# Kernel tuning notes

Hardware: AMD Instinct MI355X
Metric: run time of the kernel (lower is better)

The kernel has to match this reference:

```python
import jax, jax.numpy as jnp
import numpy as np

N = 4096
D_IN = 1024
D_OUT = 512
DENSITY = 0.005
LRELU_ALPHA = 0.2  # tf.nn.leaky_relu default


def _make_adj(key):
    # sparse binary adjacency, symmetric, with self-loops (dense 0/1 float mask)
    a = (jax.random.uniform(key, (N, N)) < DENSITY).astype(jnp.float32)
    a = jnp.maximum(a, a.T)
    a = jnp.maximum(a, jnp.eye(N, dtype=jnp.float32))
    return a


def setup_inputs() -> dict:
    key = jax.random.key(0)
    ks = jax.random.split(key, 7)
    x = jax.random.normal(ks[0], (N, D_IN), dtype=jnp.float32)
    adj = _make_adj(ks[1])
    # glorot-ish scales
    Wf = jax.random.normal(ks[2], (D_IN, D_OUT), dtype=jnp.float32) * (1.0 / np.sqrt(D_IN))
    a1 = jax.random.normal(ks[3], (D_OUT, 1), dtype=jnp.float32) * (1.0 / np.sqrt(D_OUT))
    b1 = jnp.zeros((1,), dtype=jnp.float32)
    a2 = jax.random.normal(ks[4], (D_OUT, 1), dtype=jnp.float32) * (1.0 / np.sqrt(D_OUT))
    b2 = jnp.zeros((1,), dtype=jnp.float32)
    W = jax.random.normal(ks[5], (D_IN, D_OUT), dtype=jnp.float32) * (1.0 / np.sqrt(D_IN))
    return {"x": x, "adj": adj, "Wf": Wf, "a1": a1, "b1": b1, "a2": a2, "b2": b2, "W": W}


def reference(x, adj, Wf, a1, b1, a2, b2, W):
    # dropout = 0 (inference) -> identity; coef dropout skipped for determinism
    mask = adj != 0.0
    # conv1d(kernel=1) == pointwise linear
    seq_fts = x @ Wf                      # [N, D_OUT]
    f1 = seq_fts @ a1 + b1                # [N, 1]
    f2 = seq_fts @ a2 + b2                # [N, 1]
    # sparse logits: adj_ij * f1_i + adj_ij * f2_j on edges
    logits = adj * f1 + adj * f2.T        # [N, N]
    lrelu = jnp.where(logits >= 0, logits, LRELU_ALPHA * logits)
    # sparse softmax over edge entries per row
    masked = jnp.where(mask, lrelu, -jnp.inf)
    coefs = jax.nn.softmax(masked, axis=1)
    coefs = jnp.where(mask, coefs, 0.0)
    # symmetrize: (coefs + coefs^T)/2
    coefs = (coefs + coefs.T) * 0.5
    # coefs_I = diag(rowsum^0) = I  (pow(x,0)==1)
    coefs_mat = coefs + jnp.eye(N, dtype=coefs.dtype)
    rowsum = jnp.sum(coefs_mat, axis=1, keepdims=True)   # [N,1], >= 1
    d_inv_sqrt = rowsum ** -0.5
    d_inv_inverse = d_inv_sqrt ** -1.0
    inf_int = jnp.isinf(d_inv_sqrt).astype(jnp.float32)
    d = (d_inv_inverse + inf_int) ** -1.0 - inf_int
    d = jnp.sum(d, axis=1)                # [N]
    d_mat = jnp.diag(d)                   # [N,N] diagonal matrix
    # NOTE: original uses ELEMENTWISE multiply with the diag matrix (faithful):
    support_mat = (coefs_mat * d_mat).T * d_mat   # effectively diagonal
    pre_sup = x @ W                       # [N, D_OUT]
    out = support_mat @ pre_sup           # [N, D_OUT]
    return jax.nn.relu(out)
```

## Files before the change

kernel.cpp:

```cpp
#include <hip/hip_runtime.h>
#include <stdint.h>
#include <math.h>

#define NN 4096
#define DIN 1024
#define DOUT 512
#define ALPHA 0.2f

typedef __attribute__((ext_vector_type(8))) short short8;
typedef __attribute__((ext_vector_type(4))) float f32x4;

__device__ __forceinline__ unsigned short f2bf(float f) {
    uint32_t u = __float_as_uint(f);
    u += 0x7fffu + ((u >> 16) & 1u);
    return (unsigned short)(u >> 16);
}

__device__ __forceinline__ void async16(const void* g, void* l) {
    __builtin_amdgcn_global_load_lds(
        (const __attribute__((address_space(1))) uint32_t*)g,
        (__attribute__((address_space(3))) uint32_t*)l, 16, 0, 0);
}

__global__ __launch_bounds__(256) void k_wa(const float* __restrict__ Wf,
                                            const float* __restrict__ a1,
                                            const float* __restrict__ a2,
                                            float* __restrict__ wa1,
                                            float* __restrict__ wa2) {
    int row  = blockIdx.x * 4 + (threadIdx.x >> 6);
    int lane = threadIdx.x & 63;
    const float* wr = Wf + (size_t)row * DOUT;
    float s1 = 0.f, s2 = 0.f;
    for (int k = lane; k < DOUT; k += 64) {
        float w = wr[k];
        s1 += w * a1[k];
        s2 += w * a2[k];
    }
    for (int off = 32; off; off >>= 1) {
        s1 += __shfl_down(s1, off);
        s2 += __shfl_down(s2, off);
    }
    if (lane == 0) { wa1[row] = s1; wa2[row] = s2; }
}

__global__ __launch_bounds__(256) void k_maskfx(const float* __restrict__ adj,
    const float* __restrict__ x, const float* __restrict__ W,
    const float* __restrict__ wa1, const float* __restrict__ wa2,
    const float* __restrict__ b1, const float* __restrict__ b2,
    float* __restrict__ f1, float* __restrict__ f2,
    unsigned short* __restrict__ xb, unsigned short* __restrict__ wt,
    unsigned short* __restrict__ bits16) {
    int tid = threadIdx.x;
    if (blockIdx.x < 2048) {
        int row0 = blockIdx.x * 2;
        const float4* a0 = (const float4*)(adj + (size_t)row0 * NN);
        const float4* a1v = (const float4*)(adj + (size_t)(row0 + 1) * NN);
        float4 v0 = a0[tid];        float4 v1 = a0[tid + 256];
        float4 v2 = a0[tid + 512];  float4 v3 = a0[tid + 768];
        float4 v4 = a1v[tid];       float4 v5 = a1v[tid + 256];
        float4 v6 = a1v[tid + 512]; float4 v7 = a1v[tid + 768];
        __builtin_amdgcn_sched_barrier(0);
        unsigned int m0 = 0, m1 = 0;
#define MB(M, V, J)                                            \
        M |= (((V).x != 0.f) ? 1u : 0u) << (4 * (J));          \
        M |= (((V).y != 0.f) ? 1u : 0u) << (4 * (J) + 1);      \
        M |= (((V).z != 0.f) ? 1u : 0u) << (4 * (J) + 2);      \
        M |= (((V).w != 0.f) ? 1u : 0u) << (4 * (J) + 3);
        MB(m0, v0, 0) MB(m0, v1, 1) MB(m0, v2, 2) MB(m0, v3, 3)
        MB(m1, v4, 0) MB(m1, v5, 1) MB(m1, v6, 2) MB(m1, v7, 3)
#undef MB
        bits16[(size_t)row0 * 256 + tid]       = (unsigned short)m0;
        bits16[(size_t)row0 * 256 + 256 + tid] = (unsigned short)m1;
    } else if (blockIdx.x < 3072) {
        int row  = (blockIdx.x - 2048) * 4 + (tid >> 6);
        int lane = tid & 63;
        const float* xr = x + (size_t)row * DIN + lane * 16;
        float xv[16];
        *(float4*)&xv[0]  = *(const float4*)(xr);
        *(float4*)&xv[4]  = *(const float4*)(xr + 4);
        *(float4*)&xv[8]  = *(const float4*)(xr + 8);
        *(float4*)&xv[12] = *(const float4*)(xr + 12);
        __builtin_amdgcn_sched_barrier(0);
        const float* w1 = wa1 + lane * 16;
        const float* w2 = wa2 + lane * 16;
        float s1 = 0.f, s2 = 0.f;
#pragma unroll
        for (int j = 0; j < 16; ++j) {
            s1 += xv[j] * w1[j];
            s2 += xv[j] * w2[j];
        }
        union { unsigned short u[8]; uint4 q; } pk0, pk1;
#pragma unroll
        for (int j = 0; j < 8; ++j) { pk0.u[j] = f2bf(xv[j]); pk1.u[j] = f2bf(xv[8 + j]); }
        int sw = (row >> 1) & 3;
        int g0 = lane * 2, g1 = lane * 2 + 1;
        int p0 = (g0 & ~3) | ((g0 & 3) ^ sw);
        int p1 = (g1 & ~3) | ((g1 & 3) ^ sw);
        unsigned short* xrow = xb + (size_t)row * DIN;
        *(uint4*)(xrow + p0 * 8) = pk0.q;
        *(uint4*)(xrow + p1 * 8) = pk1.q;
        for (int off = 32; off; off >>= 1) {
            s1 += __shfl_down(s1, off);
            s2 += __shfl_down(s2, off);
        }
        if (lane == 0) { f1[row] = s1 + b1[0]; f2[row] = s2 + b2[0]; }
    } else {
        int idx = blockIdx.x - 3072;
        int bx = idx & 7, gy = idx >> 3;
        int n = bx * 64 + (tid & 63);
        int g = gy * 4 + (tid >> 6);
        float v[8];
#pragma unroll
        for (int j = 0; j < 8; ++j) v[j] = W[(size_t)(g * 8 + j) * DOUT + n];
        union { unsigned short u[8]; uint4 q; } pk;
#pragma unroll
        for (int j = 0; j < 8; ++j) pk.u[j] = f2bf(v[j]);
        int sw = (n >> 1) & 3;
        int p  = (g & ~3) | ((g & 3) ^ sw);
        *(uint4*)(wt + (size_t)n * DIN + p * 8) = pk.q;
    }
}

__global__ __launch_bounds__(256) void k_z(const unsigned long long* __restrict__ bits,
                                           const float* __restrict__ f1,
                                           const float* __restrict__ f2,
                                           float* __restrict__ rZ_out) {
    int row  = blockIdx.x * 4 + (threadIdx.x >> 6);
    int lane = threadIdx.x & 63;
    unsigned long long w = bits[(size_t)row * 64 + lane];
    float f1r = f1[row];
    float z = 0.f;
    while (w) {
        int b = __builtin_ctzll(w);
        w &= w - 1;
        int j = 16 * lane + 4 * (b >> 4) + 1024 * ((b >> 2) & 3) + (b & 3);
        float l = f1r + f2[j];
        z += __expf((l >= 0.f) ? l : ALPHA * l);
    }
    for (int off = 32; off; off >>= 1) z += __shfl_down(z, off);
    if (lane == 0) rZ_out[row] = 1.0f / z;
}

__global__ __launch_bounds__(256) void k_s(const unsigned long long* __restrict__ bits,
                                           const float* __restrict__ f1,
                                           const float* __restrict__ f2,
                                           const float* __restrict__ rZ,
                                           float* __restrict__ s_out) {
    int row  = blockIdx.x * 4 + (threadIdx.x >> 6);
    int lane = threadIdx.x & 63;
    unsigned long long w = bits[(size_t)row * 64 + lane];
    float f2r = f2[row];
    float sum = 0.f;
    while (w) {
        int b = __builtin_ctzll(w);
        w &= w - 1;
        int j = 16 * lane + 4 * (b >> 4) + 1024 * ((b >> 2) & 3) + (b & 3);
        float l = f1[j] + f2r;
        float e = (l >= 0.f) ? l : ALPHA * l;
        sum += __expf(e) * rZ[j];
    }
    for (int off = 32; off; off >>= 1) sum += __shfl_down(sum, off);
    if (lane == 0) {
        float l   = f1[row] + f2r;
        float e   = (l >= 0.f) ? l : ALPHA * l;
        float cjj = __expf(e) * rZ[row];
        s_out[row] = (cjj + 1.0f) / (1.5f + 0.5f * sum);
    }
}

__global__ __launch_bounds__(256) void k_gemm(const unsigned short* __restrict__ xb,
                                              const unsigned short* __restrict__ wt,
                                              const float* __restrict__ s,
                                              float* __restrict__ out) {
    __shared__ __align__(16) unsigned short As[3][64][32];
    __shared__ __align__(16) unsigned short Bs[3][64][32];
    int lid = blockIdx.y * gridDim.x + blockIdx.x;
    int xcd = lid & 7, idx = lid >> 3;
    int by = xcd * 8 + (idx & 7);
    int bx = idx >> 3;
    int bm = by * 64, bn = bx * 64;

    int tid = threadIdx.x, wid = tid >> 6, lane = tid & 63;
    int wr = wid >> 1, wc = wid & 1;

    int srow = lane >> 2, sg = lane & 3;
    const unsigned short* ga0 = xb + (size_t)(bm + wid * 16 + srow) * DIN + sg * 8;
    const unsigned short* gb0 = wt + (size_t)(bn + wid * 16 + srow) * DIN + sg * 8;

    int r15 = lane & 15, gl = lane >> 4;
    int gofs = (gl ^ ((r15 >> 1) & 3)) * 8;

    f32x4 acc[2][2] = {};

#define STAGE(BUF, K0) do {                                              \
        async16(ga0 + (K0), &As[BUF][wid * 16][0]);                      \
        async16(gb0 + (K0), &Bs[BUF][wid * 16][0]);                      \
    } while (0)

#define COMPUTE(BUF) do {                                                \
        const unsigned short* pa = &As[BUF][wr * 32 + r15][gofs];        \
        const unsigned short* pb = &Bs[BUF][wc * 32 + r15][gofs];        \
        short8 af0 = *(const short8*)(pa);                               \
        short8 af1 = *(const short8*)(pa + 16 * 32);                     \
        short8 bf0 = *(const short8*)(pb);                               \
        short8 bf1 = *(const short8*)(pb + 16 * 32);                     \
        acc[0][0] = __builtin_amdgcn_mfma_f32_16x16x32_bf16(af0, bf0, acc[0][0], 0, 0, 0); \
        acc[0][1] = __builtin_amdgcn_mfma_f32_16x16x32_bf16(af0, bf1, acc[0][1], 0, 0, 0); \
        acc[1][0] = __builtin_amdgcn_mfma_f32_16x16x32_bf16(af1, bf0, acc[1][0], 0, 0, 0); \
        acc[1][1] = __builtin_amdgcn_mfma_f32_16x16x32_bf16(af1, bf1, acc[1][1], 0, 0, 0); \
    } while (0)

#define WAITBAR(N) do {                                                  \
        asm volatile("s_waitcnt vmcnt(" #N ")" ::: "memory");            \
        __builtin_amdgcn_sched_barrier(0);                               \
        __builtin_amdgcn_s_barrier();                                    \
        __builtin_amdgcn_sched_barrier(0);                               \
    } while (0)

    STAGE(0, 0);
    STAGE(1, 32);
    for (int t = 0; t < 30; ++t) {
        WAITBAR(2);
        COMPUTE(t % 3);
        STAGE((t + 2) % 3, (t + 2) * 32);
    }
    WAITBAR(2);
    COMPUTE(0);
    WAITBAR(0);
    COMPUTE(1);

#pragma unroll
    for (int mi = 0; mi < 2; ++mi) {
        int crow0 = bm + wr * 32 + mi * 16 + gl * 4;
#pragma unroll
        for (int ni = 0; ni < 2; ++ni) {
            int ccol = bn + wc * 32 + ni * 16 + r15;
#pragma unroll
            for (int r = 0; r < 4; ++r) {
                int row = crow0 + r;
                float v = acc[mi][ni][r] * s[row];
                out[(size_t)row * DOUT + ccol] = fmaxf(v, 0.f);
            }
        }
    }
#undef STAGE
#undef COMPUTE
#undef WAITBAR
}

extern "C" void kernel_launch(void* const* d_in, const int* in_sizes, int n_in,
                              void* d_out, int out_size, void* d_ws, size_t ws_size,
                              hipStream_t stream) {
    const float* x   = (const float*)d_in[0];
    const float* adj = (const float*)d_in[1];
    const float* Wf  = (const float*)d_in[2];
    const float* a1  = (const float*)d_in[3];
    const float* b1  = (const float*)d_in[4];
    const float* a2  = (const float*)d_in[5];
    const float* b2  = (const float*)d_in[6];
    const float* W   = (const float*)d_in[7];
    float* out = (float*)d_out;

    char* w = (char*)d_ws;
    float* wa1 = (float*)(w + 0);
    float* wa2 = (float*)(w + 4096);
    float* f1  = (float*)(w + 16384);
    float* f2  = (float*)(w + 32768);
    float* rZ  = (float*)(w + 49152);
    float* s   = (float*)(w + 65536);
    unsigned short* bits16 = (unsigned short*)(w + 98304);
    unsigned short* xb = (unsigned short*)(w + 2195456);
    unsigned short* wt = (unsigned short*)(w + 10584064);

    k_wa<<<256, 256, 0, stream>>>(Wf, a1, a2, wa1, wa2);
    k_maskfx<<<3328, 256, 0, stream>>>(adj, x, W, wa1, wa2, b1, b2,
                                       f1, f2, xb, wt, bits16);
    k_z<<<1024, 256, 0, stream>>>((const unsigned long long*)bits16, f1, f2, rZ);
    k_s<<<1024, 256, 0, stream>>>((const unsigned long long*)bits16, f1, f2, rZ, s);
    dim3 gg(8, 64);
    k_gemm<<<gg, 256, 0, stream>>>(xb, wt, s, out);
}
```

Measured before the change: 43.75 us.

## Fuse softmax normalizer and column sum, regroup prep kernels

Merges the k_wa computation into the adjacency-mask and W-transpose prep kernel, and splits the x projection into its own kernel. The two row kernels (normalizer Z, then column sum) are replaced by one kernel, one block per column j. It recomputes each neighbor i's softmax normalizer on the fly, saving a launch and the rZ buffer. This adds redundant work: each row's Z is recomputed once for every neighbor, roughly 40 times, in exchange for fewer launches.

```diff
diff --git a/kernel.cpp b/kernel.cpp
--- a/kernel.cpp
+++ b/kernel.cpp
@@ -22,34 +22,11 @@
         (__attribute__((address_space(3))) uint32_t*)l, 16, 0, 0);
 }
 
-__global__ __launch_bounds__(256) void k_wa(const float* __restrict__ Wf,
-                                            const float* __restrict__ a1,
-                                            const float* __restrict__ a2,
-                                            float* __restrict__ wa1,
-                                            float* __restrict__ wa2) {
-    int row  = blockIdx.x * 4 + (threadIdx.x >> 6);
-    int lane = threadIdx.x & 63;
-    const float* wr = Wf + (size_t)row * DOUT;
-    float s1 = 0.f, s2 = 0.f;
-    for (int k = lane; k < DOUT; k += 64) {
-        float w = wr[k];
-        s1 += w * a1[k];
-        s2 += w * a2[k];
-    }
-    for (int off = 32; off; off >>= 1) {
-        s1 += __shfl_down(s1, off);
-        s2 += __shfl_down(s2, off);
-    }
-    if (lane == 0) { wa1[row] = s1; wa2[row] = s2; }
-}
-
-__global__ __launch_bounds__(256) void k_maskfx(const float* __restrict__ adj,
-    const float* __restrict__ x, const float* __restrict__ W,
-    const float* __restrict__ wa1, const float* __restrict__ wa2,
-    const float* __restrict__ b1, const float* __restrict__ b2,
-    float* __restrict__ f1, float* __restrict__ f2,
-    unsigned short* __restrict__ xb, unsigned short* __restrict__ wt,
-    unsigned short* __restrict__ bits16) {
+__global__ __launch_bounds__(256) void k_prep3(const float* __restrict__ adj,
+    const float* __restrict__ W, const float* __restrict__ Wf,
+    const float* __restrict__ a1, const float* __restrict__ a2,
+    unsigned short* __restrict__ wt, float* __restrict__ wa1,
+    float* __restrict__ wa2, unsigned short* __restrict__ bits16) {
     int tid = threadIdx.x;
     if (blockIdx.x < 2048) {
         int row0 = blockIdx.x * 2;
@@ -71,41 +48,8 @@
 #undef MB
         bits16[(size_t)row0 * 256 + tid]       = (unsigned short)m0;
         bits16[(size_t)row0 * 256 + 256 + tid] = (unsigned short)m1;
-    } else if (blockIdx.x < 3072) {
-        int row  = (blockIdx.x - 2048) * 4 + (tid >> 6);
-        int lane = tid & 63;
-        const float* xr = x + (size_t)row * DIN + lane * 16;
-        float xv[16];
-        *(float4*)&xv[0]  = *(const float4*)(xr);
-        *(float4*)&xv[4]  = *(const float4*)(xr + 4);
-        *(float4*)&xv[8]  = *(const float4*)(xr + 8);
-        *(float4*)&xv[12] = *(const float4*)(xr + 12);
-        __builtin_amdgcn_sched_barrier(0);
-        const float* w1 = wa1 + lane * 16;
-        const float* w2 = wa2 + lane * 16;
-        float s1 = 0.f, s2 = 0.f;
-#pragma unroll
-        for (int j = 0; j < 16; ++j) {
-            s1 += xv[j] * w1[j];
-            s2 += xv[j] * w2[j];
-        }
-        union { unsigned short u[8]; uint4 q; } pk0, pk1;
-#pragma unroll
-        for (int j = 0; j < 8; ++j) { pk0.u[j] = f2bf(xv[j]); pk1.u[j] = f2bf(xv[8 + j]); }
-        int sw = (row >> 1) & 3;
-        int g0 = lane * 2, g1 = lane * 2 + 1;
-        int p0 = (g0 & ~3) | ((g0 & 3) ^ sw);
-        int p1 = (g1 & ~3) | ((g1 & 3) ^ sw);
-        unsigned short* xrow = xb + (size_t)row * DIN;
-        *(uint4*)(xrow + p0 * 8) = pk0.q;
-        *(uint4*)(xrow + p1 * 8) = pk1.q;
-        for (int off = 32; off; off >>= 1) {
-            s1 += __shfl_down(s1, off);
-            s2 += __shfl_down(s2, off);
-        }
-        if (lane == 0) { f1[row] = s1 + b1[0]; f2[row] = s2 + b2[0]; }
-    } else {
-        int idx = blockIdx.x - 3072;
+    } else if (blockIdx.x < 2304) {
+        int idx = blockIdx.x - 2048;
         int bx = idx & 7, gy = idx >> 3;
         int n = bx * 64 + (tid & 63);
         int g = gy * 4 + (tid >> 6);
@@ -118,53 +62,108 @@
         int sw = (n >> 1) & 3;
         int p  = (g & ~3) | ((g & 3) ^ sw);
         *(uint4*)(wt + (size_t)n * DIN + p * 8) = pk.q;
-    }
-}
-
-__global__ __launch_bounds__(256) void k_z(const unsigned long long* __restrict__ bits,
-                                           const float* __restrict__ f1,
-                                           const float* __restrict__ f2,
-                                           float* __restrict__ rZ_out) {
+    } else {
+        int row  = (blockIdx.x - 2304) * 4 + (tid >> 6);
+        int lane = tid & 63;
+        const float* wr = Wf + (size_t)row * DOUT;
+        float s1 = 0.f, s2 = 0.f;
+        for (int k = lane; k < DOUT; k += 64) {
+            float w = wr[k];
+            s1 += w * a1[k];
+            s2 += w * a2[k];
+        }
+        for (int off = 32; off; off >>= 1) {
+            s1 += __shfl_down(s1, off);
+            s2 += __shfl_down(s2, off);
+        }
+        if (lane == 0) { wa1[row] = s1; wa2[row] = s2; }
+    }
+}
+
+__global__ __launch_bounds__(256) void k_fx(const float* __restrict__ x,
+    const float* __restrict__ wa1, const float* __restrict__ wa2,
+    const float* __restrict__ b1, const float* __restrict__ b2,
+    float* __restrict__ f1, float* __restrict__ f2,
+    unsigned short* __restrict__ xb) {
     int row  = blockIdx.x * 4 + (threadIdx.x >> 6);
     int lane = threadIdx.x & 63;
-    unsigned long long w = bits[(size_t)row * 64 + lane];
-    float f1r = f1[row];
-    float z = 0.f;
-    while (w) {
-        int b = __builtin_ctzll(w);
-        w &= w - 1;
-        int j = 16 * lane + 4 * (b >> 4) + 1024 * ((b >> 2) & 3) + (b & 3);
-        float l = f1r + f2[j];
-        z += __expf((l >= 0.f) ? l : ALPHA * l);
-    }
-    for (int off = 32; off; off >>= 1) z += __shfl_down(z, off);
-    if (lane == 0) rZ_out[row] = 1.0f / z;
-}
-
-__global__ __launch_bounds__(256) void k_s(const unsigned long long* __restrict__ bits,
-                                           const float* __restrict__ f1,
-                                           const float* __restrict__ f2,
-                                           const float* __restrict__ rZ,
-                                           float* __restrict__ s_out) {
-    int row  = blockIdx.x * 4 + (threadIdx.x >> 6);
-    int lane = threadIdx.x & 63;
-    unsigned long long w = bits[(size_t)row * 64 + lane];
-    float f2r = f2[row];
-    float sum = 0.f;
-    while (w) {
-        int b = __builtin_ctzll(w);
-        w &= w - 1;
-        int j = 16 * lane + 4 * (b >> 4) + 1024 * ((b >> 2) & 3) + (b & 3);
-        float l = f1[j] + f2r;
-        float e = (l >= 0.f) ? l : ALPHA * l;
-        sum += __expf(e) * rZ[j];
-    }
-    for (int off = 32; off; off >>= 1) sum += __shfl_down(sum, off);
+    const float* xr = x + (size_t)row * DIN + lane * 16;
+    float xv[16];
+    *(float4*)&xv[0]  = *(const float4*)(xr);
+    *(float4*)&xv[4]  = *(const float4*)(xr + 4);
+    *(float4*)&xv[8]  = *(const float4*)(xr + 8);
+    *(float4*)&xv[12] = *(const float4*)(xr + 12);
+    __builtin_amdgcn_sched_barrier(0);
+    const float* w1 = wa1 + lane * 16;
+    const float* w2 = wa2 + lane * 16;
+    float s1 = 0.f, s2 = 0.f;
+#pragma unroll
+    for (int j = 0; j < 16; ++j) {
+        s1 += xv[j] * w1[j];
+        s2 += xv[j] * w2[j];
+    }
+    union { unsigned short u[8]; uint4 q; } pk0, pk1;
+#pragma unroll
+    for (int j = 0; j < 8; ++j) { pk0.u[j] = f2bf(xv[j]); pk1.u[j] = f2bf(xv[8 + j]); }
+    int sw = (row >> 1) & 3;
+    int g0 = lane * 2, g1 = lane * 2 + 1;
+    int p0 = (g0 & ~3) | ((g0 & 3) ^ sw);
+    int p1 = (g1 & ~3) | ((g1 & 3) ^ sw);
+    unsigned short* xrow = xb + (size_t)row * DIN;
+    *(uint4*)(xrow + p0 * 8) = pk0.q;
+    *(uint4*)(xrow + p1 * 8) = pk1.q;
+    for (int off = 32; off; off >>= 1) {
+        s1 += __shfl_down(s1, off);
+        s2 += __shfl_down(s2, off);
+    }
+    if (lane == 0) { f1[row] = s1 + b1[0]; f2[row] = s2 + b2[0]; }
+}
+
+__global__ __launch_bounds__(256) void k_zs(const unsigned long long* __restrict__ bits,
+                                            const float* __restrict__ f1,
+                                            const float* __restrict__ f2,
+                                            float* __restrict__ s_out) {
+    int j = blockIdx.x;
+    int tid = threadIdx.x, wid = tid >> 6, lane = tid & 63;
+    float f2j = f2[j];
+    __shared__ float cpart[4];
+    __shared__ float rzj_sh;
+    float csum = 0.f;
+    float rzj = 0.f;
+    for (int q = 0; q < 16; ++q) {
+        int wl = wid * 16 + q;
+        unsigned long long wj = bits[(size_t)j * 64 + wl];
+        while (wj) {
+            int b = __builtin_ctzll(wj); wj &= wj - 1;
+            int i = 16 * wl + 4 * (b >> 4) + 1024 * ((b >> 2) & 3) + (b & 3);
+            float f1i = f1[i];
+            unsigned long long wi = bits[(size_t)i * 64 + lane];
+            float z = 0.f;
+            while (wi) {
+                int bb = __builtin_ctzll(wi); wi &= wi - 1;
+                int k = 16 * lane + 4 * (bb >> 4) + 1024 * ((bb >> 2) & 3) + (bb & 3);
+                float l = f1i + f2[k];
+                z += __expf((l >= 0.f) ? l : ALPHA * l);
+            }
+#pragma unroll
+            for (int off = 32; off; off >>= 1) z += __shfl_xor(z, off);
+            float rzi = 1.0f / z;
+            float lij = f1i + f2j;
+            csum += __expf((lij >= 0.f) ? lij : ALPHA * lij) * rzi;
+            if (i == j) rzj = rzi;
+        }
+    }
     if (lane == 0) {
-        float l   = f1[row] + f2r;
-        float e   = (l >= 0.f) ? l : ALPHA * l;
-        float cjj = __expf(e) * rZ[row];
-        s_out[row] = (cjj + 1.0f) / (1.5f + 0.5f * sum);
+        cpart[wid] = csum;
+        if (rzj != 0.f) rzj_sh = rzj;
+    }
+    __syncthreads();
+    if (tid == 0) {
+        float colsum = cpart[0] + cpart[1] + cpart[2] + cpart[3];
+        float ljj = f1[j] + f2j;
+        float e   = (ljj >= 0.f) ? ljj : ALPHA * ljj;
+        float cjj = __expf(e) * rzj_sh;
+        s_out[j] = (cjj + 1.0f) / (1.5f + 0.5f * colsum);
     }
 }
 
@@ -266,17 +265,14 @@
     float* wa2 = (float*)(w + 4096);
     float* f1  = (float*)(w + 16384);
     float* f2  = (float*)(w + 32768);
-    float* rZ  = (float*)(w + 49152);
     float* s   = (float*)(w + 65536);
     unsigned short* bits16 = (unsigned short*)(w + 98304);
     unsigned short* xb = (unsigned short*)(w + 2195456);
     unsigned short* wt = (unsigned short*)(w + 10584064);
 
-    k_wa<<<256, 256, 0, stream>>>(Wf, a1, a2, wa1, wa2);
-    k_maskfx<<<3328, 256, 0, stream>>>(adj, x, W, wa1, wa2, b1, b2,
-                                       f1, f2, xb, wt, bits16);
-    k_z<<<1024, 256, 0, stream>>>((const unsigned long long*)bits16, f1, f2, rZ);
-    k_s<<<1024, 256, 0, stream>>>((const unsigned long long*)bits16, f1, f2, rZ, s);
+    k_prep3<<<2560, 256, 0, stream>>>(adj, W, Wf, a1, a2, wt, wa1, wa2, bits16);
+    k_fx<<<1024, 256, 0, stream>>>(x, wa1, wa2, b1, b2, f1, f2, xb);
+    k_zs<<<4096, 256, 0, stream>>>((const unsigned long long*)bits16, f1, f2, s);
     dim3 gg(8, 64);
     k_gemm<<<gg, 256, 0, stream>>>(xb, wt, s, out);
 }
```

After: 91.10 us. 2.08x slower.

## Fuse row-scale computation into GEMM and regroup prep kernels

Applied to the files above, without the earlier changes.

Moves the per-row scale computation (old k_s) into the GEMM kernel's prologue, where each block computes the scales for its 64 rows into LDS while the first async tile loads are in flight. The prep work is also regrouped: the adjacency bitmask, the W transpose and the Wf·a projection now share one kernel, and the x conversion with f1/f2 runs in its own kernel. This removes one launch and the global round-trip for s, but each row's scale is now recomputed by all 8 column blocks, which lengthens the GEMM prologue.

```diff
diff --git a/kernel.cpp b/kernel.cpp
--- a/kernel.cpp
+++ b/kernel.cpp
@@ -22,34 +22,11 @@
         (__attribute__((address_space(3))) uint32_t*)l, 16, 0, 0);
 }
 
-__global__ __launch_bounds__(256) void k_wa(const float* __restrict__ Wf,
-                                            const float* __restrict__ a1,
-                                            const float* __restrict__ a2,
-                                            float* __restrict__ wa1,
-                                            float* __restrict__ wa2) {
-    int row  = blockIdx.x * 4 + (threadIdx.x >> 6);
-    int lane = threadIdx.x & 63;
-    const float* wr = Wf + (size_t)row * DOUT;
-    float s1 = 0.f, s2 = 0.f;
-    for (int k = lane; k < DOUT; k += 64) {
-        float w = wr[k];
-        s1 += w * a1[k];
-        s2 += w * a2[k];
-    }
-    for (int off = 32; off; off >>= 1) {
-        s1 += __shfl_down(s1, off);
-        s2 += __shfl_down(s2, off);
-    }
-    if (lane == 0) { wa1[row] = s1; wa2[row] = s2; }
-}
-
-__global__ __launch_bounds__(256) void k_maskfx(const float* __restrict__ adj,
-    const float* __restrict__ x, const float* __restrict__ W,
-    const float* __restrict__ wa1, const float* __restrict__ wa2,
-    const float* __restrict__ b1, const float* __restrict__ b2,
-    float* __restrict__ f1, float* __restrict__ f2,
-    unsigned short* __restrict__ xb, unsigned short* __restrict__ wt,
-    unsigned short* __restrict__ bits16) {
+__global__ __launch_bounds__(256) void k_prep3(const float* __restrict__ adj,
+    const float* __restrict__ W, const float* __restrict__ Wf,
+    const float* __restrict__ a1, const float* __restrict__ a2,
+    unsigned short* __restrict__ wt, float* __restrict__ wa1,
+    float* __restrict__ wa2, unsigned short* __restrict__ bits16) {
     int tid = threadIdx.x;
     if (blockIdx.x < 2048) {
         int row0 = blockIdx.x * 2;
@@ -71,41 +48,8 @@
 #undef MB
         bits16[(size_t)row0 * 256 + tid]       = (unsigned short)m0;
         bits16[(size_t)row0 * 256 + 256 + tid] = (unsigned short)m1;
-    } else if (blockIdx.x < 3072) {
-        int row  = (blockIdx.x - 2048) * 4 + (tid >> 6);
-        int lane = tid & 63;
-        const float* xr = x + (size_t)row * DIN + lane * 16;
-        float xv[16];
-        *(float4*)&xv[0]  = *(const float4*)(xr);
-        *(float4*)&xv[4]  = *(const float4*)(xr + 4);
-        *(float4*)&xv[8]  = *(const float4*)(xr + 8);
-        *(float4*)&xv[12] = *(const float4*)(xr + 12);
-        __builtin_amdgcn_sched_barrier(0);
-        const float* w1 = wa1 + lane * 16;
-        const float* w2 = wa2 + lane * 16;
-        float s1 = 0.f, s2 = 0.f;
-#pragma unroll
-        for (int j = 0; j < 16; ++j) {
-            s1 += xv[j] * w1[j];
-            s2 += xv[j] * w2[j];
-        }
-        union { unsigned short u[8]; uint4 q; } pk0, pk1;
-#pragma unroll
-        for (int j = 0; j < 8; ++j) { pk0.u[j] = f2bf(xv[j]); pk1.u[j] = f2bf(xv[8 + j]); }
-        int sw = (row >> 1) & 3;
-        int g0 = lane * 2, g1 = lane * 2 + 1;
-        int p0 = (g0 & ~3) | ((g0 & 3) ^ sw);
-        int p1 = (g1 & ~3) | ((g1 & 3) ^ sw);
-        unsigned short* xrow = xb + (size_t)row * DIN;
-        *(uint4*)(xrow + p0 * 8) = pk0.q;
-        *(uint4*)(xrow + p1 * 8) = pk1.q;
-        for (int off = 32; off; off >>= 1) {
-            s1 += __shfl_down(s1, off);
-            s2 += __shfl_down(s2, off);
-        }
-        if (lane == 0) { f1[row] = s1 + b1[0]; f2[row] = s2 + b2[0]; }
-    } else {
-        int idx = blockIdx.x - 3072;
+    } else if (blockIdx.x < 2304) {
+        int idx = blockIdx.x - 2048;
         int bx = idx & 7, gy = idx >> 3;
         int n = bx * 64 + (tid & 63);
         int g = gy * 4 + (tid >> 6);
@@ -118,7 +62,61 @@
         int sw = (n >> 1) & 3;
         int p  = (g & ~3) | ((g & 3) ^ sw);
         *(uint4*)(wt + (size_t)n * DIN + p * 8) = pk.q;
-    }
+    } else {
+        int row  = (blockIdx.x - 2304) * 4 + (tid >> 6);
+        int lane = tid & 63;
+        const float* wr = Wf + (size_t)row * DOUT;
+        float s1 = 0.f, s2 = 0.f;
+        for (int k = lane; k < DOUT; k += 64) {
+            float w = wr[k];
+            s1 += w * a1[k];
+            s2 += w * a2[k];
+        }
+        for (int off = 32; off; off >>= 1) {
+            s1 += __shfl_down(s1, off);
+            s2 += __shfl_down(s2, off);
+        }
+        if (lane == 0) { wa1[row] = s1; wa2[row] = s2; }
+    }
+}
+
+__global__ __launch_bounds__(256) void k_fx(const float* __restrict__ x,
+    const float* __restrict__ wa1, const float* __restrict__ wa2,
+    const float* __restrict__ b1, const float* __restrict__ b2,
+    float* __restrict__ f1, float* __restrict__ f2,
+    unsigned short* __restrict__ xb) {
+    int row  = blockIdx.x * 4 + (threadIdx.x >> 6);
+    int lane = threadIdx.x & 63;
+    const float* xr = x + (size_t)row * DIN + lane * 16;
+    float xv[16];
+    *(float4*)&xv[0]  = *(const float4*)(xr);
+    *(float4*)&xv[4]  = *(const float4*)(xr + 4);
+    *(float4*)&xv[8]  = *(const float4*)(xr + 8);
+    *(float4*)&xv[12] = *(const float4*)(xr + 12);
+    __builtin_amdgcn_sched_barrier(0);
+    const float* w1 = wa1 + lane * 16;
+    const float* w2 = wa2 + lane * 16;
+    float s1 = 0.f, s2 = 0.f;
+#pragma unroll
+    for (int j = 0; j < 16; ++j) {
+        s1 += xv[j] * w1[j];
+        s2 += xv[j] * w2[j];
+    }
+    union { unsigned short u[8]; uint4 q; } pk0, pk1;
+#pragma unroll
+    for (int j = 0; j < 8; ++j) { pk0.u[j] = f2bf(xv[j]); pk1.u[j] = f2bf(xv[8 + j]); }
+    int sw = (row >> 1) & 3;
+    int g0 = lane * 2, g1 = lane * 2 + 1;
+    int p0 = (g0 & ~3) | ((g0 & 3) ^ sw);
+    int p1 = (g1 & ~3) | ((g1 & 3) ^ sw);
+    unsigned short* xrow = xb + (size_t)row * DIN;
+    *(uint4*)(xrow + p0 * 8) = pk0.q;
+    *(uint4*)(xrow + p1 * 8) = pk1.q;
+    for (int off = 32; off; off >>= 1) {
+        s1 += __shfl_down(s1, off);
+        s2 += __shfl_down(s2, off);
+    }
+    if (lane == 0) { f1[row] = s1 + b1[0]; f2[row] = s2 + b2[0]; }
 }
 
 __global__ __launch_bounds__(256) void k_z(const unsigned long long* __restrict__ bits,
@@ -141,39 +139,16 @@
     if (lane == 0) rZ_out[row] = 1.0f / z;
 }
 
-__global__ __launch_bounds__(256) void k_s(const unsigned long long* __restrict__ bits,
-                                           const float* __restrict__ f1,
-                                           const float* __restrict__ f2,
-                                           const float* __restrict__ rZ,
-                                           float* __restrict__ s_out) {
-    int row  = blockIdx.x * 4 + (threadIdx.x >> 6);
-    int lane = threadIdx.x & 63;
-    unsigned long long w = bits[(size_t)row * 64 + lane];
-    float f2r = f2[row];
-    float sum = 0.f;
-    while (w) {
-        int b = __builtin_ctzll(w);
-        w &= w - 1;
-        int j = 16 * lane + 4 * (b >> 4) + 1024 * ((b >> 2) & 3) + (b & 3);
-        float l = f1[j] + f2r;
-        float e = (l >= 0.f) ? l : ALPHA * l;
-        sum += __expf(e) * rZ[j];
-    }
-    for (int off = 32; off; off >>= 1) sum += __shfl_down(sum, off);
-    if (lane == 0) {
-        float l   = f1[row] + f2r;
-        float e   = (l >= 0.f) ? l : ALPHA * l;
-        float cjj = __expf(e) * rZ[row];
-        s_out[row] = (cjj + 1.0f) / (1.5f + 0.5f * sum);
-    }
-}
-
 __global__ __launch_bounds__(256) void k_gemm(const unsigned short* __restrict__ xb,
                                               const unsigned short* __restrict__ wt,
-                                              const float* __restrict__ s,
+                                              const unsigned long long* __restrict__ bits,
+                                              const float* __restrict__ f1,
+                                              const float* __restrict__ f2,
+                                              const float* __restrict__ rZ,
                                               float* __restrict__ out) {
     __shared__ __align__(16) unsigned short As[3][64][32];
     __shared__ __align__(16) unsigned short Bs[3][64][32];
+    __shared__ float s_lds[64];
     int lid = blockIdx.y * gridDim.x + blockIdx.x;
     int xcd = lid & 7, idx = lid >> 3;
     int by = xcd * 8 + (idx & 7);
@@ -219,6 +194,31 @@
 
     STAGE(0, 0);
     STAGE(1, 32);
+
+    for (int r = 0; r < 16; ++r) {
+        int lrow = wid * 16 + r;
+        int row  = bm + lrow;
+        unsigned long long w = bits[(size_t)row * 64 + lane];
+        float f2r = f2[row];
+        float sum = 0.f;
+        while (w) {
+            int bb = __builtin_ctzll(w);
+            w &= w - 1;
+            int j = 16 * lane + 4 * (bb >> 4) + 1024 * ((bb >> 2) & 3) + (bb & 3);
+            float l = f1[j] + f2r;
+            float e = (l >= 0.f) ? l : ALPHA * l;
+            sum += __expf(e) * rZ[j];
+        }
+        for (int off = 32; off; off >>= 1) sum += __shfl_down(sum, off);
+        if (lane == 0) {
+            float l   = f1[row] + f2r;
+            float e   = (l >= 0.f) ? l : ALPHA * l;
+            float cjj = __expf(e) * rZ[row];
+            s_lds[lrow] = (cjj + 1.0f) / (1.5f + 0.5f * sum);
+        }
+    }
+    asm volatile("s_waitcnt lgkmcnt(0)" ::: "memory");
+
     for (int t = 0; t < 30; ++t) {
         WAITBAR(2);
         COMPUTE(t % 3);
@@ -231,15 +231,15 @@
 
 #pragma unroll
     for (int mi = 0; mi < 2; ++mi) {
-        int crow0 = bm + wr * 32 + mi * 16 + gl * 4;
+        int lrow0 = wr * 32 + mi * 16 + gl * 4;
 #pragma unroll
         for (int ni = 0; ni < 2; ++ni) {
             int ccol = bn + wc * 32 + ni * 16 + r15;
 #pragma unroll
             for (int r = 0; r < 4; ++r) {
-                int row = crow0 + r;
-                float v = acc[mi][ni][r] * s[row];
-                out[(size_t)row * DOUT + ccol] = fmaxf(v, 0.f);
+                int lrow = lrow0 + r;
+                float v = acc[mi][ni][r] * s_lds[lrow];
+                out[(size_t)(bm + lrow) * DOUT + ccol] = fmaxf(v, 0.f);
             }
         }
     }
@@ -267,16 +267,14 @@
     float* f1  = (float*)(w + 16384);
     float* f2  = (float*)(w + 32768);
     float* rZ  = (float*)(w + 49152);
-    float* s   = (float*)(w + 65536);
     unsigned short* bits16 = (unsigned short*)(w + 98304);
     unsigned short* xb = (unsigned short*)(w + 2195456);
     unsigned short* wt = (unsigned short*)(w + 10584064);
 
-    k_wa<<<256, 256, 0, stream>>>(Wf, a1, a2, wa1, wa2);
-    k_maskfx<<<3328, 256, 0, stream>>>(adj, x, W, wa1, wa2, b1, b2,
-                                       f1, f2, xb, wt, bits16);
+    k_prep3<<<2560, 256, 0, stream>>>(adj, W, Wf, a1, a2, wt, wa1, wa2, bits16);
+    k_fx<<<1024, 256, 0, stream>>>(x, wa1, wa2, b1, b2, f1, f2, xb);
     k_z<<<1024, 256, 0, stream>>>((const unsigned long long*)bits16, f1, f2, rZ);
-    k_s<<<1024, 256, 0, stream>>>((const unsigned long long*)bits16, f1, f2, rZ, s);
     dim3 gg(8, 64);
-    k_gemm<<<gg, 256, 0, stream>>>(xb, wt, s, out);
-}
+    k_gemm<<<gg, 256, 0, stream>>>(xb, wt, (const unsigned long long*)bits16,
+                                   f1, f2, rZ, out);
+}
```

New measurement: 58.26 us. 33.2% more time.

## Split preprocessing into two kernels overlapping mask build with weight prep

Applied to the files above, without the earlier changes.

The standalone Wf·a reduction kernel and the combined mask/fx kernel are regrouped into two kernels. The first builds the adjacency bitmask for half the rows alongside the W transpose and the wa reduction. The second handles the other half of the mask alongside the x projection and bf16 conversion that depend on wa. Each mask block now processes four rows instead of two. The aim is to hide the small dependent kernel behind bandwidth-heavy adjacency reads and cut one serialized launch, at the cost of more registers per thread in the mask path.

```diff
diff --git a/kernel.cpp b/kernel.cpp
--- a/kernel.cpp
+++ b/kernel.cpp
@@ -22,13 +22,36 @@
         (__attribute__((address_space(3))) uint32_t*)l, 16, 0, 0);
 }
 
-__global__ __launch_bounds__(256) void k_wa(const float* __restrict__ Wf,
-                                            const float* __restrict__ a1,
-                                            const float* __restrict__ a2,
-                                            float* __restrict__ wa1,
-                                            float* __restrict__ wa2) {
-    int row  = blockIdx.x * 4 + (threadIdx.x >> 6);
-    int lane = threadIdx.x & 63;
+__device__ __forceinline__ void mask4(const float* __restrict__ adj,
+                                      unsigned short* __restrict__ bits16,
+                                      int row0, int tid) {
+    const float* a0 = adj + (size_t)row0 * NN;
+    float4 v[16];
+#pragma unroll
+    for (int r = 0; r < 4; ++r)
+#pragma unroll
+        for (int i = 0; i < 4; ++i)
+            v[r * 4 + i] = ((const float4*)(a0 + (size_t)r * NN))[tid + 256 * i];
+    __builtin_amdgcn_sched_barrier(0);
+    unsigned int m[4] = {0, 0, 0, 0};
+#pragma unroll
+    for (int r = 0; r < 4; ++r)
+#pragma unroll
+        for (int i = 0; i < 4; ++i) {
+            float4 q = v[r * 4 + i];
+            m[r] |= ((q.x != 0.f) ? 1u : 0u) << (4 * i);
+            m[r] |= ((q.y != 0.f) ? 1u : 0u) << (4 * i + 1);
+            m[r] |= ((q.z != 0.f) ? 1u : 0u) << (4 * i + 2);
+            m[r] |= ((q.w != 0.f) ? 1u : 0u) << (4 * i + 3);
+        }
+#pragma unroll
+    for (int r = 0; r < 4; ++r)
+        bits16[(size_t)(row0 + r) * 256 + tid] = (unsigned short)m[r];
+}
+
+__device__ __forceinline__ void wa_row(const float* __restrict__ Wf,
+    const float* __restrict__ a1, const float* __restrict__ a2,
+    float* __restrict__ wa1, float* __restrict__ wa2, int row, int lane) {
     const float* wr = Wf + (size_t)row * DOUT;
     float s1 = 0.f, s2 = 0.f;
     for (int k = lane; k < DOUT; k += 64) {
@@ -43,81 +66,86 @@
     if (lane == 0) { wa1[row] = s1; wa2[row] = s2; }
 }
 
-__global__ __launch_bounds__(256) void k_maskfx(const float* __restrict__ adj,
-    const float* __restrict__ x, const float* __restrict__ W,
+__device__ __forceinline__ void wt_unit(const float* __restrict__ W,
+    unsigned short* __restrict__ wt, int idx, int tid) {
+    int bx = idx & 7, gy = idx >> 3;
+    int n = bx * 64 + (tid & 63);
+    int g = gy * 4 + (tid >> 6);
+    float v[8];
+#pragma unroll
+    for (int j = 0; j < 8; ++j) v[j] = W[(size_t)(g * 8 + j) * DOUT + n];
+    union { unsigned short u[8]; uint4 q; } pk;
+#pragma unroll
+    for (int j = 0; j < 8; ++j) pk.u[j] = f2bf(v[j]);
+    int sw = (n >> 1) & 3;
+    int p  = (g & ~3) | ((g & 3) ^ sw);
+    *(uint4*)(wt + (size_t)n * DIN + p * 8) = pk.q;
+}
+
+__device__ __forceinline__ void fx_row(const float* __restrict__ x,
     const float* __restrict__ wa1, const float* __restrict__ wa2,
     const float* __restrict__ b1, const float* __restrict__ b2,
     float* __restrict__ f1, float* __restrict__ f2,
-    unsigned short* __restrict__ xb, unsigned short* __restrict__ wt,
-    unsigned short* __restrict__ bits16) {
-    int tid = threadIdx.x;
-    if (blockIdx.x < 2048) {
-        int row0 = blockIdx.x * 2;
-        const float4* a0 = (const float4*)(adj + (size_t)row0 * NN);
-        const float4* a1v = (const float4*)(adj + (size_t)(row0 + 1) * NN);
-        float4 v0 = a0[tid];        float4 v1 = a0[tid + 256];
-        float4 v2 = a0[tid + 512];  float4 v3 = a0[tid + 768];
-        float4 v4 = a1v[tid];       float4 v5 = a1v[tid + 256];
-        float4 v6 = a1v[tid + 512]; float4 v7 = a1v[tid + 768];
-        __builtin_amdgcn_sched_barrier(0);
-        unsigned int m0 = 0, m1 = 0;
-#define MB(M, V, J)                                            \
-        M |= (((V).x != 0.f) ? 1u : 0u) << (4 * (J));          \
-        M |= (((V).y != 0.f) ? 1u : 0u) << (4 * (J) + 1);      \
-        M |= (((V).z != 0.f) ? 1u : 0u) << (4 * (J) + 2);      \
-        M |= (((V).w != 0.f) ? 1u : 0u) << (4 * (J) + 3);
-        MB(m0, v0, 0) MB(m0, v1, 1) MB(m0, v2, 2) MB(m0, v3, 3)
-        MB(m1, v4, 0) MB(m1, v5, 1) MB(m1, v6, 2) MB(m1, v7, 3)
-#undef MB
-        bits16[(size_t)row0 * 256 + tid]       = (unsigned short)m0;
-        bits16[(size_t)row0 * 256 + 256 + tid] = (unsigned short)m1;
-    } else if (blockIdx.x < 3072) {
-        int row  = (blockIdx.x - 2048) * 4 + (tid >> 6);
-        int lane = tid & 63;
-        const float* xr = x + (size_t)row * DIN + lane * 16;
-        float xv[16];
-        *(float4*)&xv[0]  = *(const float4*)(xr);
-        *(float4*)&xv[4]  = *(const float4*)(xr + 4);
-        *(float4*)&xv[8]  = *(const float4*)(xr + 8);
-        *(float4*)&xv[12] = *(const float4*)(xr + 12);
-        __builtin_amdgcn_sched_barrier(0);
-        const float* w1 = wa1 + lane * 16;
-        const float* w2 = wa2 + lane * 16;
-        float s1 = 0.f, s2 = 0.f;
-#pragma unroll
-        for (int j = 0; j < 16; ++j) {
-            s1 += xv[j] * w1[j];
-            s2 += xv[j] * w2[j];
-        }
-        union { unsigned short u[8]; uint4 q; } pk0, pk1;
-#pragma unroll
-        for (int j = 0; j < 8; ++j) { pk0.u[j] = f2bf(xv[j]); pk1.u[j] = f2bf(xv[8 + j]); }
-        int sw = (row >> 1) & 3;
-        int g0 = lane * 2, g1 = lane * 2 + 1;
-        int p0 = (g0 & ~3) | ((g0 & 3) ^ sw);
-        int p1 = (g1 & ~3) | ((g1 & 3) ^ sw);
-        unsigned short* xrow = xb + (size_t)row * DIN;
-        *(uint4*)(xrow + p0 * 8) = pk0.q;
-        *(uint4*)(xrow + p1 * 8) = pk1.q;
-        for (int off = 32; off; off >>= 1) {
-            s1 += __shfl_down(s1, off);
-            s2 += __shfl_down(s2, off);
-        }
-        if (lane == 0) { f1[row] = s1 + b1[0]; f2[row] = s2 + b2[0]; }
+    unsigned short* __restrict__ xb, int row, int lane) {
+    const float* xr = x + (size_t)row * DIN + lane * 16;
+    float xv[16];
+    *(float4*)&xv[0]  = *(const float4*)(xr);
+    *(float4*)&xv[4]  = *(const float4*)(xr + 4);
+    *(float4*)&xv[8]  = *(const float4*)(xr + 8);
+    *(float4*)&xv[12] = *(const float4*)(xr + 12);
+    __builtin_amdgcn_sched_barrier(0);
+    const float* w1 = wa1 + lane * 16;
+    const float* w2 = wa2 + lane * 16;
+    float s1 = 0.f, s2 = 0.f;
+#pragma unroll
+    for (int j = 0; j < 16; ++j) {
+        s1 += xv[j] * w1[j];
+        s2 += xv[j] * w2[j];
+    }
+    union { unsigned short u[8]; uint4 q; } pk0, pk1;
+#pragma unroll
+    for (int j = 0; j < 8; ++j) { pk0.u[j] = f2bf(xv[j]); pk1.u[j] = f2bf(xv[8 + j]); }
+    int sw = (row >> 1) & 3;
+    int g0 = lane * 2, g1 = lane * 2 + 1;
+    int p0 = (g0 & ~3) | ((g0 & 3) ^ sw);
+    int p1 = (g1 & ~3) | ((g1 & 3) ^ sw);
+    unsigned short* xrow = xb + (size_t)row * DIN;
+    *(uint4*)(xrow + p0 * 8) = pk0.q;
+    *(uint4*)(xrow + p1 * 8) = pk1.q;
+    for (int off = 32; off; off >>= 1) {
+        s1 += __shfl_down(s1, off);
+        s2 += __shfl_down(s2, off);
+    }
+    if (lane == 0) { f1[row] = s1 + b1[0]; f2[row] = s2 + b2[0]; }
+}
+
+__global__ __launch_bounds__(256) void k_p1(const float* __restrict__ adj,
+    const float* __restrict__ W, const float* __restrict__ Wf,
+    const float* __restrict__ a1, const float* __restrict__ a2,
+    unsigned short* __restrict__ wt, float* __restrict__ wa1,
+    float* __restrict__ wa2, unsigned short* __restrict__ bits16) {
+    int tid = threadIdx.x, b = blockIdx.x;
+    if (b < 512) {
+        mask4(adj, bits16, b * 4, tid);
+    } else if (b < 768) {
+        wt_unit(W, wt, b - 512, tid);
     } else {
-        int idx = blockIdx.x - 3072;
-        int bx = idx & 7, gy = idx >> 3;
-        int n = bx * 64 + (tid & 63);
-        int g = gy * 4 + (tid >> 6);
-        float v[8];
-#pragma unroll
-        for (int j = 0; j < 8; ++j) v[j] = W[(size_t)(g * 8 + j) * DOUT + n];
-        union { unsigned short u[8]; uint4 q; } pk;
-#pragma unroll
-        for (int j = 0; j < 8; ++j) pk.u[j] = f2bf(v[j]);
-        int sw = (n >> 1) & 3;
-        int p  = (g & ~3) | ((g & 3) ^ sw);
-        *(uint4*)(wt + (size_t)n * DIN + p * 8) = pk.q;
+        wa_row(Wf, a1, a2, wa1, wa2, (b - 768) * 4 + (tid >> 6), tid & 63);
+    }
+}
+
+__global__ __launch_bounds__(256) void k_p2(const float* __restrict__ adj,
+    const float* __restrict__ x,
+    const float* __restrict__ wa1, const float* __restrict__ wa2,
+    const float* __restrict__ b1, const float* __restrict__ b2,
+    float* __restrict__ f1, float* __restrict__ f2,
+    unsigned short* __restrict__ xb, unsigned short* __restrict__ bits16) {
+    int tid = threadIdx.x, b = blockIdx.x;
+    if (b < 512) {
+        mask4(adj, bits16, 2048 + b * 4, tid);
+    } else {
+        fx_row(x, wa1, wa2, b1, b2, f1, f2, xb,
+               (b - 512) * 4 + (tid >> 6), tid & 63);
     }
 }
 
@@ -272,9 +300,8 @@
     unsigned short* xb = (unsigned short*)(w + 2195456);
     unsigned short* wt = (unsigned short*)(w + 10584064);
 
-    k_wa<<<256, 256, 0, stream>>>(Wf, a1, a2, wa1, wa2);
-    k_maskfx<<<3328, 256, 0, stream>>>(adj, x, W, wa1, wa2, b1, b2,
-                                       f1, f2, xb, wt, bits16);
+    k_p1<<<1024, 256, 0, stream>>>(adj, W, Wf, a1, a2, wt, wa1, wa2, bits16);
+    k_p2<<<1536, 256, 0, stream>>>(adj, x, wa1, wa2, b1, b2, f1, f2, xb, bits16);
     k_z<<<1024, 256, 0, stream>>>((const unsigned long long*)bits16, f1, f2, rZ);
     k_s<<<1024, 256, 0, stream>>>((const unsigned long long*)bits16, f1, f2, rZ, s);
     dim3 gg(8, 64);
```

Result: no change. 43.43 us (-0.7%).
